# Optimization experiments

Hardware: AMD Instinct MI355X
Metric: run time of the kernel (lower is better)

## Reference

```python
import math
import jax, jax.numpy as jnp
import numpy as np

HIDDEN = 128
NLAYERS = 3
MAXLEN = 4096
B = 64
NEG_SLOPE = 0.2

def compute_patch_scheme(maxlen, nlayers):
    patch_lens, patch_nums = [], []
    cur = maxlen
    for i in range(nlayers):
        r = nlayers - i
        pn = math.ceil(cur ** (1.0 / r))
        pl = math.ceil(cur / pn)
        apn = math.ceil(cur / pl)
        patch_lens.append(pl)
        patch_nums.append(apn)
        cur = apn
    return patch_lens, patch_nums

PATCH_LENS, PATCH_NUMS = compute_patch_scheme(MAXLEN, NLAYERS)

def build_edges(pl):
    # chain edges both directions + self loops (exactly as build_patch_edge_index)
    e = []
    for i in range(pl - 1):
        e.append((i, i + 1))
        e.append((i + 1, i))
    for i in range(pl):
        e.append((i, i))
    e = np.asarray(e, dtype=np.int32)
    return jnp.asarray(e[:, 0]), jnp.asarray(e[:, 1])

EDGES = [build_edges(pl) for pl in PATCH_LENS]

def gat_layer(xp, src, dst, n, W, a_src, a_dst, b):
    # xp: [G, n, d]. pyg GATConv, heads=1: h = x @ W.T (lin has no bias)
    h = jnp.einsum('gnd,ed->gne', xp, W)          # [G, n, d]
    s = h @ a_src                                  # [G, n] alpha_src per node
    t = h @ a_dst                                  # [G, n] alpha_dst per node
    e = jax.nn.leaky_relu(s[:, src] + t[:, dst], NEG_SLOPE).T   # [E, G]
    emax = jax.ops.segment_max(e, dst, num_segments=n)          # [n, G]
    ex = jnp.exp(e - emax[dst])                                  # [E, G]
    denom = jax.ops.segment_sum(ex, dst, num_segments=n)        # [n, G]
    alpha = (ex / denom[dst]).T                                  # [G, E]
    msg = h[:, src, :] * alpha[..., None]                        # [G, E, d]
    out = jax.ops.segment_sum(msg.transpose(1, 0, 2), dst, num_segments=n)  # [n, G, d]
    return out.transpose(1, 0, 2) + b                            # [G, n, d]

def _forward(x, lengths, params):
    Bsz, d, _ = x.shape
    for i in range(NLAYERS):
        pl = PATCH_LENS[i]
        T = x.shape[2]
        pad = (-T) % pl
        if pad:
            x = jnp.pad(x, ((0, 0), (0, 0), (0, pad)))
        P = x.shape[2] // pl
        xp = x.reshape(Bsz, d, P, pl).transpose(0, 2, 3, 1).reshape(Bsz * P, pl, d)
        mask = (jnp.arange(P * pl)[None, :] < lengths[:, None]).reshape(Bsz, P, pl).astype(x.dtype)
        src, dst = EDGES[i]
        W, a_s, a_d, b = params[i]
        out = gat_layer(xp, src, dst, pl, W, a_s, a_d, b).reshape(Bsz, P, pl, d)
        m = mask[..., None]                               # [B, P, pl, 1]
        feat = (out * m).sum(axis=2) / jnp.maximum(m.sum(axis=2), 1.0)  # masked mean -> [B, P, d]
        x = feat.transpose(0, 2, 1)                       # [B, d, P]
        lengths = jnp.full((Bsz,), P, dtype=lengths.dtype)
    if x.shape[-1] == 1:  # torch .squeeze(-1)
        x = x[..., 0]
    return x

def setup_inputs() -> dict:
    key = jax.random.key(0)
    ks = jax.random.split(key, 2 + 4 * NLAYERS)
    d = HIDDEN
    scale = 1.0 / math.sqrt(d)  # glorot-ish scaling keeps attention logits sane
    inp = {
        'x': jax.random.normal(ks[0], (B, d, MAXLEN), dtype=jnp.float32),
        'lengths': jax.random.randint(ks[1], (B,), 1, MAXLEN + 1, dtype=jnp.int32),
    }
    for i in range(NLAYERS):
        k0, k1, k2, _ = ks[2 + 4 * i], ks[3 + 4 * i], ks[4 + 4 * i], ks[5 + 4 * i]
        inp[f'W{i}'] = jax.random.normal(k0, (d, d), dtype=jnp.float32) * scale
        inp[f'asrc{i}'] = jax.random.normal(k1, (d,), dtype=jnp.float32) * scale
        inp[f'adst{i}'] = jax.random.normal(k2, (d,), dtype=jnp.float32) * scale
        inp[f'bias{i}'] = jnp.zeros((d,), dtype=jnp.float32)
    return inp

def reference(x, lengths, W0, asrc0, adst0, bias0, W1, asrc1, adst1, bias1, W2, asrc2, adst2, bias2):
    params = [(W0, asrc0, adst0, bias0), (W1, asrc1, adst1, bias1), (W2, asrc2, adst2, bias2)]
    return _forward(x, lengths, params)
```

## Files before the change

kernel.cpp:

```cpp
#include <hip/hip_runtime.h>

#define NEG_SLOPE 0.2f

#define OFF_U   0
#define OFF_WT  1024
#define OFF_X1  50176

__device__ __forceinline__ float lrelu(float z) { return z >= 0.f ? z : NEG_SLOPE * z; }

__device__ __forceinline__ unsigned short f2bf(float f) {
  unsigned u = __float_as_uint(f);
  u += 0x7FFFu + ((u >> 16) & 1u);
  return (unsigned short)(u >> 16);
}

__global__ __launch_bounds__(256) void setup_kernel(
    const float* __restrict__ W0, const float* __restrict__ as0, const float* __restrict__ ad0,
    const float* __restrict__ W1, const float* __restrict__ as1, const float* __restrict__ ad1,
    const float* __restrict__ W2, const float* __restrict__ as2, const float* __restrict__ ad2,
    float* __restrict__ ws) {
  __shared__ float tile[8][132];
  const int bid = blockIdx.x;
  const int l = bid >> 4, sub = bid & 15;
  const int tid = threadIdx.x;
  const float* W = (l == 0) ? W0 : (l == 1) ? W1 : W2;
  float* WT = ws + OFF_WT + l * 16384;
  const int e0 = sub * 8;

#pragma unroll
  for (int i = 0; i < 4; ++i) {
    const int idx = i * 256 + tid;
    tile[idx >> 7][idx & 127] = W[(e0 + (idx >> 7)) * 128 + (idx & 127)];
  }
  __syncthreads();
#pragma unroll
  for (int i = 0; i < 4; ++i) {
    const int idx = i * 256 + tid;
    const int d = idx >> 3, j = idx & 7;
    WT[d * 128 + e0 + j] = tile[j][d];
  }
  if (sub == 0) {
    const float* av = (tid < 128) ? ((l == 0) ? as0 : (l == 1) ? as1 : as2)
                                  : ((l == 0) ? ad0 : (l == 1) ? ad1 : ad2);
    const int d = tid & 127;
    float acc = 0.f;
#pragma unroll 8
    for (int e = 0; e < 128; ++e) acc += av[e] * W[e * 128 + d];
    ws[OFF_U + l * 256 + tid] = acc;
  }
}

__global__ __launch_bounds__(512, 4) void l0_kernel(
    const float* __restrict__ x, const int* __restrict__ lengths,
    const float* __restrict__ uvec, const float* __restrict__ WT0,
    const float* __restrict__ b0, float* __restrict__ x1) {
  __shared__ unsigned short xs[128 * 264];
  __shared__ float red[2048];
  __shared__ float sA[256], tA[256];
  __shared__ float u_sh[256];

  const int tid  = threadIdx.x;
  const int bid  = blockIdx.x;
  const int b    = bid >> 4;
  const int p    = bid & 15;
  const int lane = tid & 63;
  const int wave = __builtin_amdgcn_readfirstlane(tid >> 6);

  if (tid < 256) u_sh[tid] = uvec[tid];
  __syncthreads();

  const float* xb = x + ((size_t)b * 128) * 4096 + p * 256;
  float s0 = 0.f, s1 = 0.f, s2 = 0.f, s3 = 0.f;
  float t0 = 0.f, t1 = 0.f, t2 = 0.f, t3 = 0.f;
#pragma unroll 8
  for (int it = 0; it < 16; ++it) {
    const int d = it * 8 + wave;
    const float4 v = *(const float4*)(xb + (size_t)d * 4096 + lane * 4);
    const float us = u_sh[d];
    const float ud = u_sh[128 + d];
    s0 += v.x * us; s1 += v.y * us; s2 += v.z * us; s3 += v.w * us;
    t0 += v.x * ud; t1 += v.y * ud; t2 += v.z * ud; t3 += v.w * ud;
    ushort4 pk;
    pk.x = f2bf(v.x); pk.y = f2bf(v.y); pk.z = f2bf(v.z); pk.w = f2bf(v.w);
    *(ushort4*)(&xs[d * 264 + lane * 4]) = pk;
  }

  const int n4 = lane * 4;
  if (wave >= 4) *(float4*)(&red[(wave - 4) * 256 + n4])   = make_float4(s0, s1, s2, s3);
  else           *(float4*)(&red[1024 + wave * 256 + n4])  = make_float4(t0, t1, t2, t3);
  __syncthreads();
  if (wave < 4) {
    float4 r = *(float4*)(&red[wave * 256 + n4]);
    r.x += s0; r.y += s1; r.z += s2; r.w += s3;
    *(float4*)(&red[wave * 256 + n4]) = r;
  } else {
    float4 r = *(float4*)(&red[1024 + (wave - 4) * 256 + n4]);
    r.x += t0; r.y += t1; r.z += t2; r.w += t3;
    *(float4*)(&red[1024 + (wave - 4) * 256 + n4]) = r;
  }
  __syncthreads();
  if (tid < 256) {
    sA[tid] = red[tid] + red[256 + tid] + red[512 + tid] + red[768 + tid];
  } else {
    const int n = tid - 256;
    tA[n] = red[1024 + n] + red[1280 + n] + red[1536 + n] + red[1792 + n];
  }
  __syncthreads();

  const int len = lengths[b];

  if (tid < 256) {
    const int j = tid;
    const float tj = tA[j];
    const float ls = lrelu(sA[j] + tj);
    const float lm = (j > 0)   ? lrelu(sA[j - 1] + tj) : -1e30f;
    const float lp = (j < 255) ? lrelu(sA[j + 1] + tj) : -1e30f;
    const float mx = fmaxf(ls, fmaxf(lm, lp));
    const float em = (j > 0)   ? __expf(lm - mx) : 0.f;
    const float es = __expf(ls - mx);
    const float ep = (j < 255) ? __expf(lp - mx) : 0.f;
    const float vj = ((p * 256 + j) < len) ? 1.f : 0.f;
    const float sc = vj / (em + es + ep);
    red[j] = em * sc;
    red[256 + j] = es * sc;
    red[512 + j] = ep * sc;
  }
  __syncthreads();

  if (tid < 256) {
    const int n = tid;
    float w = red[256 + n];
    if (n < 255) w += red[n + 1];
    if (n > 0)   w += red[512 + n - 1];
    red[768 + n] = w;
  }
  __syncthreads();

  {
    const int d = tid >> 2, q = tid & 3;
    float acc = 0.f;
#pragma unroll 8
    for (int j = 0; j < 32; ++j) {
      const int jj = (j + d + q * 8) & 31;
      const int n  = q * 64 + jj * 2;
      const unsigned pair = *(const unsigned*)(&xs[d * 264 + n]);
      const float f0 = __uint_as_float(pair << 16);
      const float f1 = __uint_as_float(pair & 0xFFFF0000u);
      const float2 w2 = *(const float2*)(&red[768 + n]);
      acc += w2.x * f0 + w2.y * f1;
    }
    red[1024 + tid] = acc;
  }
  __syncthreads();

  if (tid < 128) {
    const float4 r = *(const float4*)(&red[1024 + tid * 4]);
    sA[tid] = r.x + r.y + r.z + r.w;
  }
  __syncthreads();

  {
    const int e = tid & 127, eh = tid >> 7;
    float acc = 0.f;
#pragma unroll 8
    for (int k = 0; k < 32; ++k) {
      const int d = eh * 32 + k;
      acc += sA[d] * WT0[d * 128 + e];
    }
    red[eh * 128 + e] = acc;
  }
  __syncthreads();

  if (tid < 128) {
    const int e = tid;
    const int rem = len - p * 256;
    const int cnt = rem < 0 ? 0 : (rem > 256 ? 256 : rem);
    float o = 0.f;
    if (cnt > 0)
      o = (red[e] + red[128 + e] + red[256 + e] + red[384 + e]) / (float)cnt + b0[e];
    x1[(size_t)(b * 128 + e) * 16 + p] = o;
  }
}

__global__ __launch_bounds__(128) void l12_kernel(
    const float* __restrict__ x1, const float* __restrict__ u1,
    const float* __restrict__ WT1, const float* __restrict__ b1,
    const float* __restrict__ WT2, const float* __restrict__ b2,
    float* __restrict__ out) {
  __shared__ float xg[128][4];
  __shared__ float stp[8][128];
  __shared__ float sA[4], tA[4], am[4], asf[4], ap[4], w4[4];
  __shared__ float x2l[128];

  const int tid = threadIdx.x;
  const int bid = blockIdx.x;
  const int b = bid >> 2, p = bid & 3;

  const int d = tid;
  const float4 v = *(const float4*)(x1 + (size_t)(b * 128 + d) * 16 + p * 4);
  *(float4*)(&xg[d][0]) = v;
  const float us = u1[d], ud = u1[128 + d];
  stp[0][d] = v.x * us; stp[1][d] = v.y * us; stp[2][d] = v.z * us; stp[3][d] = v.w * us;
  stp[4][d] = v.x * ud; stp[5][d] = v.y * ud; stp[6][d] = v.z * ud; stp[7][d] = v.w * ud;
  __syncthreads();

  if (tid < 8) {
    float acc = 0.f;
    for (int k = 0; k < 128; ++k) acc += stp[tid][k];
    if (tid < 4) sA[tid] = acc; else tA[tid - 4] = acc;
  }
  __syncthreads();

  if (tid < 4) {
    const int j = tid;
    const float tj = tA[j];
    const float ls = lrelu(sA[j] + tj);
    const float lm = (j > 0) ? lrelu(sA[j - 1] + tj) : -1e30f;
    const float lp = (j < 3) ? lrelu(sA[j + 1] + tj) : -1e30f;
    const float mx = fmaxf(ls, fmaxf(lm, lp));
    const float em = (j > 0) ? __expf(lm - mx) : 0.f;
    const float es = __expf(ls - mx);
    const float ep = (j < 3) ? __expf(lp - mx) : 0.f;
    const float sc = 1.f / (em + es + ep);
    am[j] = em * sc; asf[j] = es * sc; ap[j] = ep * sc;
  }
  __syncthreads();

  if (tid < 4) {
    const int n = tid;
    float w = asf[n];
    if (n < 3) w += am[n + 1];
    if (n > 0) w += ap[n - 1];
    w4[n] = w;
  }
  __syncthreads();

  {
    const float w0 = w4[0], w1 = w4[1], w2 = w4[2], w3 = w4[3];
    float acc = 0.f;
#pragma unroll 8
    for (int dd = 0; dd < 128; ++dd) {
      const float xt = w0 * xg[dd][0] + w1 * xg[dd][1] + w2 * xg[dd][2] + w3 * xg[dd][3];
      acc += xt * WT1[dd * 128 + tid];
    }
    x2l[tid] = acc * 0.25f + b1[tid];
  }
  __syncthreads();

  {
    float acc = 0.f;
#pragma unroll 8
    for (int dd = 0; dd < 128; ++dd) acc += x2l[dd] * WT2[dd * 128 + tid];
    out[(size_t)(b * 128 + tid) * 4 + p] = acc + b2[tid];
  }
}

extern "C" void kernel_launch(void* const* d_in, const int* in_sizes, int n_in,
                              void* d_out, int out_size, void* d_ws, size_t ws_size,
                              hipStream_t stream) {
  (void)in_sizes; (void)n_in; (void)out_size; (void)ws_size;
  const float* x       = (const float*)d_in[0];
  const int*   lengths = (const int*)  d_in[1];
  const float* W0  = (const float*)d_in[2];
  const float* as0 = (const float*)d_in[3];
  const float* ad0 = (const float*)d_in[4];
  const float* b0  = (const float*)d_in[5];
  const float* W1  = (const float*)d_in[6];
  const float* as1 = (const float*)d_in[7];
  const float* ad1 = (const float*)d_in[8];
  const float* b1  = (const float*)d_in[9];
  const float* W2  = (const float*)d_in[10];
  const float* as2 = (const float*)d_in[11];
  const float* ad2 = (const float*)d_in[12];
  const float* b2  = (const float*)d_in[13];
  float* ws  = (float*)d_ws;
  float* out = (float*)d_out;

  setup_kernel<<<48, 256, 0, stream>>>(W0, as0, ad0, W1, as1, ad1, W2, as2, ad2, ws);
  l0_kernel<<<1024, 512, 0, stream>>>(x, lengths, ws + OFF_U, ws + OFF_WT, b0, ws + OFF_X1);
  l12_kernel<<<256, 128, 0, stream>>>(ws + OFF_X1, ws + OFF_U + 256,
                                      ws + OFF_WT + 16384, b1,
                                      ws + OFF_WT + 32768, b2, out);
}
```

Before: 56.98 us.

## Split layer-0 patches across two blocks and move W0 projection into layer-1/2 kernel

Layer 0 now launches twice as many 256-thread blocks, each covering half a 256-column patch. Each block keeps its x tile in registers instead of a bf16 shared-memory copy and fetches the halo columns from global memory. It emits only the attention-weighted row sum per half, and the W0 projection, bias and length normalization move into the l12 kernel, which now runs one block per batch over all 16 patches. This removes the large LDS footprint and most syncs in the memory-bound layer 0, at the cost of a much narrower 64-block tail kernel.

```diff
diff --git a/kernel.cpp b/kernel.cpp
--- a/kernel.cpp
+++ b/kernel.cpp
@@ -4,15 +4,9 @@
 
 #define OFF_U   0
 #define OFF_WT  1024
-#define OFF_X1  50176
+#define OFF_XT  50176
 
 __device__ __forceinline__ float lrelu(float z) { return z >= 0.f ? z : NEG_SLOPE * z; }
-
-__device__ __forceinline__ unsigned short f2bf(float f) {
-  unsigned u = __float_as_uint(f);
-  u += 0x7FFFu + ((u >> 16) & 1u);
-  return (unsigned short)(u >> 16);
-}
 
 __global__ __launch_bounds__(256) void setup_kernel(
     const float* __restrict__ W0, const float* __restrict__ as0, const float* __restrict__ ad0,
@@ -50,208 +44,281 @@
   }
 }
 
-__global__ __launch_bounds__(512, 4) void l0_kernel(
+__global__ __launch_bounds__(256, 4) void l0_kernel(
     const float* __restrict__ x, const int* __restrict__ lengths,
-    const float* __restrict__ uvec, const float* __restrict__ WT0,
-    const float* __restrict__ b0, float* __restrict__ x1) {
-  __shared__ unsigned short xs[128 * 264];
-  __shared__ float red[2048];
-  __shared__ float sA[256], tA[256];
+    const float* __restrict__ uvec, float* __restrict__ xt_out) {
   __shared__ float u_sh[256];
+  __shared__ float stp[4][256];
+  __shared__ float hal[4][128];
+  __shared__ float hred[4][32];
+  __shared__ float sF[132], tF[132];
+  __shared__ float am1[132], asf[132], ap1[132];
+  __shared__ float w_sh[128];
 
   const int tid  = threadIdx.x;
   const int bid  = blockIdx.x;
-  const int b    = bid >> 4;
-  const int p    = bid & 15;
+  const int b = bid >> 5;
+  const int p = (bid >> 1) & 15;
+  const int h = bid & 1;
   const int lane = tid & 63;
-  const int wave = __builtin_amdgcn_readfirstlane(tid >> 6);
-
-  if (tid < 256) u_sh[tid] = uvec[tid];
-  __syncthreads();
-
-  const float* xb = x + ((size_t)b * 128) * 4096 + p * 256;
+  const int wave = tid >> 6;
+  const int l32  = lane & 31;
+  const int hi32 = lane >> 5;
+  const int c0 = h * 128;
+
+  u_sh[tid] = uvec[tid];
+
+  const float* xb = x + ((size_t)b * 128) * 4096 + p * 256 + c0;
+  float4 xr[16];
+#pragma unroll
+  for (int it = 0; it < 16; ++it) {
+    const int d = it * 8 + wave * 2 + hi32;
+    xr[it] = *(const float4*)(xb + (size_t)d * 4096 + l32 * 4);
+  }
+  const int grp = tid >> 7;
+  const int hc = ((h == 0) ? 128 : 126) + grp;
+  const int dh = tid & 127;
+  const float hv = x[((size_t)b * 128 + dh) * 4096 + p * 256 + hc];
+
+  __syncthreads();
+
   float s0 = 0.f, s1 = 0.f, s2 = 0.f, s3 = 0.f;
   float t0 = 0.f, t1 = 0.f, t2 = 0.f, t3 = 0.f;
-#pragma unroll 8
+#pragma unroll
   for (int it = 0; it < 16; ++it) {
-    const int d = it * 8 + wave;
-    const float4 v = *(const float4*)(xb + (size_t)d * 4096 + lane * 4);
-    const float us = u_sh[d];
-    const float ud = u_sh[128 + d];
+    const int d = it * 8 + wave * 2 + hi32;
+    const float us = u_sh[d], ud = u_sh[128 + d];
+    const float4 v = xr[it];
     s0 += v.x * us; s1 += v.y * us; s2 += v.z * us; s3 += v.w * us;
     t0 += v.x * ud; t1 += v.y * ud; t2 += v.z * ud; t3 += v.w * ud;
-    ushort4 pk;
-    pk.x = f2bf(v.x); pk.y = f2bf(v.y); pk.z = f2bf(v.z); pk.w = f2bf(v.w);
-    *(ushort4*)(&xs[d * 264 + lane * 4]) = pk;
-  }
-
-  const int n4 = lane * 4;
-  if (wave >= 4) *(float4*)(&red[(wave - 4) * 256 + n4])   = make_float4(s0, s1, s2, s3);
-  else           *(float4*)(&red[1024 + wave * 256 + n4])  = make_float4(t0, t1, t2, t3);
-  __syncthreads();
-  if (wave < 4) {
-    float4 r = *(float4*)(&red[wave * 256 + n4]);
-    r.x += s0; r.y += s1; r.z += s2; r.w += s3;
-    *(float4*)(&red[wave * 256 + n4]) = r;
-  } else {
-    float4 r = *(float4*)(&red[1024 + (wave - 4) * 256 + n4]);
-    r.x += t0; r.y += t1; r.z += t2; r.w += t3;
-    *(float4*)(&red[1024 + (wave - 4) * 256 + n4]) = r;
-  }
-  __syncthreads();
-  if (tid < 256) {
-    sA[tid] = red[tid] + red[256 + tid] + red[512 + tid] + red[768 + tid];
-  } else {
-    const int n = tid - 256;
-    tA[n] = red[1024 + n] + red[1280 + n] + red[1536 + n] + red[1792 + n];
+  }
+  hal[grp * 2 + 0][dh] = hv * u_sh[dh];
+  hal[grp * 2 + 1][dh] = hv * u_sh[128 + dh];
+
+  s0 += __shfl_xor(s0, 32); s1 += __shfl_xor(s1, 32);
+  s2 += __shfl_xor(s2, 32); s3 += __shfl_xor(s3, 32);
+  t0 += __shfl_xor(t0, 32); t1 += __shfl_xor(t1, 32);
+  t2 += __shfl_xor(t2, 32); t3 += __shfl_xor(t3, 32);
+  if (hi32 == 0) {
+    const int n4 = l32 * 4;
+    stp[wave][n4] = s0; stp[wave][n4 + 1] = s1; stp[wave][n4 + 2] = s2; stp[wave][n4 + 3] = s3;
+    stp[wave][128 + n4] = t0; stp[wave][128 + n4 + 1] = t1;
+    stp[wave][128 + n4 + 2] = t2; stp[wave][128 + n4 + 3] = t3;
+  }
+  __syncthreads();
+
+  {
+    const float r = stp[0][tid] + stp[1][tid] + stp[2][tid] + stp[3][tid];
+    if (tid < 128) sF[tid + 2] = r; else tF[(tid - 128) + 2] = r;
+  }
+  if (tid < 128) {
+    const int q = tid >> 5, i = tid & 31;
+    hred[q][i] = hal[q][i] + hal[q][32 + i] + hal[q][64 + i] + hal[q][96 + i];
+  }
+  __syncthreads();
+
+  if (tid < 4) {
+    float a = 0.f;
+#pragma unroll
+    for (int i = 0; i < 32; ++i) a += hred[tid][i];
+    if (h == 0) {
+      if (tid == 0) sF[130] = a;
+      else if (tid == 1) tF[130] = a;
+      else if (tid == 2) sF[131] = a;
+    } else {
+      if (tid == 0) sF[0] = a;
+      else if (tid == 2) sF[1] = a;
+      else if (tid == 3) tF[1] = a;
+    }
   }
   __syncthreads();
 
   const int len = lengths[b];
 
-  if (tid < 256) {
-    const int j = tid;
-    const float tj = tA[j];
-    const float ls = lrelu(sA[j] + tj);
-    const float lm = (j > 0)   ? lrelu(sA[j - 1] + tj) : -1e30f;
-    const float lp = (j < 255) ? lrelu(sA[j + 1] + tj) : -1e30f;
+  if (tid <= 128) {
+    const int k = tid - (h ? 1 : 0);
+    const int a = c0 + k;
+    const float tj = tF[k + 2];
+    const float ls = lrelu(sF[k + 2] + tj);
+    const float lm = (a > 0)   ? lrelu(sF[k + 1] + tj) : -1e30f;
+    const float lp = (a < 255) ? lrelu(sF[k + 3] + tj) : -1e30f;
     const float mx = fmaxf(ls, fmaxf(lm, lp));
-    const float em = (j > 0)   ? __expf(lm - mx) : 0.f;
+    const float em = (a > 0)   ? __expf(lm - mx) : 0.f;
     const float es = __expf(ls - mx);
-    const float ep = (j < 255) ? __expf(lp - mx) : 0.f;
-    const float vj = ((p * 256 + j) < len) ? 1.f : 0.f;
+    const float ep = (a < 255) ? __expf(lp - mx) : 0.f;
+    const float vj = ((p * 256 + a) < len) ? 1.f : 0.f;
     const float sc = vj / (em + es + ep);
-    red[j] = em * sc;
-    red[256 + j] = es * sc;
-    red[512 + j] = ep * sc;
-  }
-  __syncthreads();
-
-  if (tid < 256) {
+    am1[k + 2] = em * sc; asf[k + 2] = es * sc; ap1[k + 2] = ep * sc;
+  }
+  __syncthreads();
+
+  if (tid < 128) {
     const int n = tid;
-    float w = red[256 + n];
-    if (n < 255) w += red[n + 1];
-    if (n > 0)   w += red[512 + n - 1];
-    red[768 + n] = w;
-  }
-  __syncthreads();
-
-  {
-    const int d = tid >> 2, q = tid & 3;
-    float acc = 0.f;
+    const int a = c0 + n;
+    float w = asf[n + 2];
+    if (a < 255) w += am1[n + 3];
+    if (a > 0)   w += ap1[n + 1];
+    w_sh[n] = w;
+  }
+  __syncthreads();
+
+  {
+    const float4 wv = *(const float4*)(&w_sh[l32 * 4]);
+    float* dst = xt_out + (((size_t)b * 16 + p) * 2 + h) * 128;
+#pragma unroll
+    for (int it = 0; it < 16; ++it) {
+      float a = wv.x * xr[it].x + wv.y * xr[it].y + wv.z * xr[it].z + wv.w * xr[it].w;
+      a += __shfl_xor(a, 1);  a += __shfl_xor(a, 2);  a += __shfl_xor(a, 4);
+      a += __shfl_xor(a, 8);  a += __shfl_xor(a, 16);
+      if (l32 == 0) {
+        const int d = it * 8 + wave * 2 + hi32;
+        dst[d] = a;
+      }
+    }
+  }
+}
+
+__global__ __launch_bounds__(256) void l12_kernel(
+    const float* __restrict__ xtp, const int* __restrict__ lengths,
+    const float* __restrict__ ws,
+    const float* __restrict__ b0, const float* __restrict__ b1,
+    const float* __restrict__ b2, float* __restrict__ out) {
+  __shared__ float xt[16][128];
+  __shared__ float pr[2][16][128];
+  __shared__ float feat[16][128];
+  __shared__ float spt[2][16][16];
+  __shared__ float s1[16], t1[16], am[16], asf[16], ap[16], w16[16];
+  __shared__ float rc_sh[16];
+  __shared__ float x1t[4][128];
+  __shared__ float h1[4][128];
+
+  const int tid = threadIdx.x;
+  const int b = blockIdx.x;
+  const float* WT0 = ws + OFF_WT;
+  const float* WT1 = ws + OFF_WT + 16384;
+  const float* WT2 = ws + OFF_WT + 32768;
+  const float* u1  = ws + OFF_U + 256;
+  const int len = lengths[b];
+
+#pragma unroll
+  for (int i = 0; i < 8; ++i) {
+    const int pp = i * 2 + (tid >> 7);
+    const int d = tid & 127;
+    const size_t base = (((size_t)b * 16 + pp) * 2) * 128;
+    xt[pp][d] = xtp[base + d] + xtp[base + 128 + d];
+  }
+  if (tid < 16) {
+    const int rem = len - tid * 256;
+    const int cnt = rem < 0 ? 0 : (rem > 256 ? 256 : rem);
+    rc_sh[tid] = cnt > 0 ? 1.f / (float)cnt : 0.f;
+  }
+  __syncthreads();
+
+  {
+    const int e = tid & 127, dhalf = tid >> 7;
+    float acc[16];
+#pragma unroll
+    for (int q = 0; q < 16; ++q) acc[q] = 0.f;
+#pragma unroll 4
+    for (int k = 0; k < 64; ++k) {
+      const int d = dhalf * 64 + k;
+      const float wv = WT0[d * 128 + e];
+#pragma unroll
+      for (int q = 0; q < 16; ++q) acc[q] += xt[q][d] * wv;
+    }
+#pragma unroll
+    for (int q = 0; q < 16; ++q) pr[dhalf][q][e] = acc[q];
+  }
+  __syncthreads();
+  {
+    const int e = tid & 127, ph = tid >> 7;
+    const float bb = b0[e];
+#pragma unroll
+    for (int i = 0; i < 8; ++i) {
+      const int q = ph * 8 + i;
+      const float rcv = rc_sh[q];
+      const float f = (pr[0][q][e] + pr[1][q][e]) * rcv + bb;
+      feat[q][e] = (rcv == 0.f) ? 0.f : f;
+    }
+  }
+  __syncthreads();
+
+  {
+    const int q = tid >> 4, sl = tid & 15;
+    float ps = 0.f, pt = 0.f;
+#pragma unroll
+    for (int k = 0; k < 8; ++k) {
+      const int e = sl * 8 + k;
+      const float f = feat[q][e];
+      ps += f * u1[e];
+      pt += f * u1[128 + e];
+    }
+    spt[0][q][sl] = ps; spt[1][q][sl] = pt;
+  }
+  __syncthreads();
+  if (tid < 32) {
+    const int q = tid >> 4, pp = tid & 15;
+    float a = 0.f;
+#pragma unroll
+    for (int i = 0; i < 16; ++i) a += spt[q][pp][i];
+    if (q == 0) s1[pp] = a; else t1[pp] = a;
+  }
+  __syncthreads();
+  if (tid < 16) {
+    const int jl = tid & 3;
+    const float tj = t1[tid];
+    const float ls = lrelu(s1[tid] + tj);
+    const float lm = (jl > 0) ? lrelu(s1[tid - 1] + tj) : -1e30f;
+    const float lp = (jl < 3) ? lrelu(s1[tid + 1] + tj) : -1e30f;
+    const float mx = fmaxf(ls, fmaxf(lm, lp));
+    const float em = (jl > 0) ? __expf(lm - mx) : 0.f;
+    const float es = __expf(ls - mx);
+    const float ep = (jl < 3) ? __expf(lp - mx) : 0.f;
+    const float sc = 1.f / (em + es + ep);
+    am[tid] = em * sc; asf[tid] = es * sc; ap[tid] = ep * sc;
+  }
+  __syncthreads();
+  if (tid < 16) {
+    const int jl = tid & 3;
+    float w = asf[tid];
+    if (jl < 3) w += am[tid + 1];
+    if (jl > 0) w += ap[tid - 1];
+    w16[tid] = w;
+  }
+  __syncthreads();
+#pragma unroll
+  for (int r = 0; r < 2; ++r) {
+    const int idx = r * 256 + tid;
+    const int g = idx >> 7, d = idx & 127;
+    x1t[g][d] = w16[g * 4] * feat[g * 4][d] + w16[g * 4 + 1] * feat[g * 4 + 1][d]
+              + w16[g * 4 + 2] * feat[g * 4 + 2][d] + w16[g * 4 + 3] * feat[g * 4 + 3][d];
+  }
+  __syncthreads();
+  {
+    const int e = tid & 127, gh = tid >> 7;
+    float a0 = 0.f, a1 = 0.f;
 #pragma unroll 8
-    for (int j = 0; j < 32; ++j) {
-      const int jj = (j + d + q * 8) & 31;
-      const int n  = q * 64 + jj * 2;
-      const unsigned pair = *(const unsigned*)(&xs[d * 264 + n]);
-      const float f0 = __uint_as_float(pair << 16);
-      const float f1 = __uint_as_float(pair & 0xFFFF0000u);
-      const float2 w2 = *(const float2*)(&red[768 + n]);
-      acc += w2.x * f0 + w2.y * f1;
-    }
-    red[1024 + tid] = acc;
-  }
-  __syncthreads();
-
-  if (tid < 128) {
-    const float4 r = *(const float4*)(&red[1024 + tid * 4]);
-    sA[tid] = r.x + r.y + r.z + r.w;
-  }
-  __syncthreads();
-
-  {
-    const int e = tid & 127, eh = tid >> 7;
-    float acc = 0.f;
+    for (int d = 0; d < 128; ++d) {
+      const float wv = WT1[d * 128 + e];
+      a0 += x1t[gh * 2][d] * wv;
+      a1 += x1t[gh * 2 + 1][d] * wv;
+    }
+    h1[gh * 2][e]     = a0 * 0.25f + b1[e];
+    h1[gh * 2 + 1][e] = a1 * 0.25f + b1[e];
+  }
+  __syncthreads();
+  {
+    const int e = tid & 127, gh = tid >> 7;
+    float a0 = 0.f, a1 = 0.f;
 #pragma unroll 8
-    for (int k = 0; k < 32; ++k) {
-      const int d = eh * 32 + k;
-      acc += sA[d] * WT0[d * 128 + e];
-    }
-    red[eh * 128 + e] = acc;
-  }
-  __syncthreads();
-
-  if (tid < 128) {
-    const int e = tid;
-    const int rem = len - p * 256;
-    const int cnt = rem < 0 ? 0 : (rem > 256 ? 256 : rem);
-    float o = 0.f;
-    if (cnt > 0)
-      o = (red[e] + red[128 + e] + red[256 + e] + red[384 + e]) / (float)cnt + b0[e];
-    x1[(size_t)(b * 128 + e) * 16 + p] = o;
-  }
-}
-
-__global__ __launch_bounds__(128) void l12_kernel(
-    const float* __restrict__ x1, const float* __restrict__ u1,
-    const float* __restrict__ WT1, const float* __restrict__ b1,
-    const float* __restrict__ WT2, const float* __restrict__ b2,
-    float* __restrict__ out) {
-  __shared__ float xg[128][4];
-  __shared__ float stp[8][128];
-  __shared__ float sA[4], tA[4], am[4], asf[4], ap[4], w4[4];
-  __shared__ float x2l[128];
-
-  const int tid = threadIdx.x;
-  const int bid = blockIdx.x;
-  const int b = bid >> 2, p = bid & 3;
-
-  const int d = tid;
-  const float4 v = *(const float4*)(x1 + (size_t)(b * 128 + d) * 16 + p * 4);
-  *(float4*)(&xg[d][0]) = v;
-  const float us = u1[d], ud = u1[128 + d];
-  stp[0][d] = v.x * us; stp[1][d] = v.y * us; stp[2][d] = v.z * us; stp[3][d] = v.w * us;
-  stp[4][d] = v.x * ud; stp[5][d] = v.y * ud; stp[6][d] = v.z * ud; stp[7][d] = v.w * ud;
-  __syncthreads();
-
-  if (tid < 8) {
-    float acc = 0.f;
-    for (int k = 0; k < 128; ++k) acc += stp[tid][k];
-    if (tid < 4) sA[tid] = acc; else tA[tid - 4] = acc;
-  }
-  __syncthreads();
-
-  if (tid < 4) {
-    const int j = tid;
-    const float tj = tA[j];
-    const float ls = lrelu(sA[j] + tj);
-    const float lm = (j > 0) ? lrelu(sA[j - 1] + tj) : -1e30f;
-    const float lp = (j < 3) ? lrelu(sA[j + 1] + tj) : -1e30f;
-    const float mx = fmaxf(ls, fmaxf(lm, lp));
-    const float em = (j > 0) ? __expf(lm - mx) : 0.f;
-    const float es = __expf(ls - mx);
-    const float ep = (j < 3) ? __expf(lp - mx) : 0.f;
-    const float sc = 1.f / (em + es + ep);
-    am[j] = em * sc; asf[j] = es * sc; ap[j] = ep * sc;
-  }
-  __syncthreads();
-
-  if (tid < 4) {
-    const int n = tid;
-    float w = asf[n];
-    if (n < 3) w += am[n + 1];
-    if (n > 0) w += ap[n - 1];
-    w4[n] = w;
-  }
-  __syncthreads();
-
-  {
-    const float w0 = w4[0], w1 = w4[1], w2 = w4[2], w3 = w4[3];
-    float acc = 0.f;
-#pragma unroll 8
-    for (int dd = 0; dd < 128; ++dd) {
-      const float xt = w0 * xg[dd][0] + w1 * xg[dd][1] + w2 * xg[dd][2] + w3 * xg[dd][3];
-      acc += xt * WT1[dd * 128 + tid];
-    }
-    x2l[tid] = acc * 0.25f + b1[tid];
-  }
-  __syncthreads();
-
-  {
-    float acc = 0.f;
-#pragma unroll 8
-    for (int dd = 0; dd < 128; ++dd) acc += x2l[dd] * WT2[dd * 128 + tid];
-    out[(size_t)(b * 128 + tid) * 4 + p] = acc + b2[tid];
+    for (int d = 0; d < 128; ++d) {
+      const float wv = WT2[d * 128 + e];
+      a0 += h1[gh * 2][d] * wv;
+      a1 += h1[gh * 2 + 1][d] * wv;
+    }
+    const float bb = b2[e];
+    out[((size_t)b * 128 + e) * 4 + gh * 2]     = a0 + bb;
+    out[((size_t)b * 128 + e) * 4 + gh * 2 + 1] = a1 + bb;
   }
 }
 
@@ -277,8 +344,6 @@
   float* out = (float*)d_out;
 
   setup_kernel<<<48, 256, 0, stream>>>(W0, as0, ad0, W1, as1, ad1, W2, as2, ad2, ws);
-  l0_kernel<<<1024, 512, 0, stream>>>(x, lengths, ws + OFF_U, ws + OFF_WT, b0, ws + OFF_X1);
-  l12_kernel<<<256, 128, 0, stream>>>(ws + OFF_X1, ws + OFF_U + 256,
-                                      ws + OFF_WT + 16384, b1,
-                                      ws + OFF_WT + 32768, b2, out);
+  l0_kernel<<<2048, 256, 0, stream>>>(x, lengths, ws + OFF_U, ws + OFF_XT);
+  l12_kernel<<<64, 256, 0, stream>>>(ws + OFF_XT, lengths, ws, b0, b1, b2, out);
 }
```

Result: slower. 72.67 us (+27.5%).
